# Kernel tuning notes

Measured on AMD Instinct MI355X. Metric: run time of the kernel, lower is better.

Reference implementation:

```python
import jax, jax.numpy as jnp
import numpy as np

N, INPUTDIM, OUTDIM, GRIDSIZE = 32768, 64, 256, 32


def setup_inputs() -> dict:
    key = jax.random.key(0)
    k1, k2 = jax.random.split(key)
    x = jax.random.normal(k1, (N, INPUTDIM), dtype=jnp.float32)
    # xavier_uniform over tensor of shape (2, outdim, inputdim, gridsize):
    # fan_in = inputdim*gridsize, fan_out = outdim*gridsize (torch treats dim0=fan_out-ish,
    # but exact init scale is irrelevant for correctness; use a matching uniform range)
    fan_in = INPUTDIM * GRIDSIZE
    fan_out = OUTDIM * GRIDSIZE
    bound = float(np.sqrt(6.0 / (fan_in + fan_out)))
    fouriercoeffs = jax.random.uniform(
        k2, (2, OUTDIM, INPUTDIM, GRIDSIZE), dtype=jnp.float32,
        minval=-bound, maxval=bound)
    bias = jnp.zeros((1, OUTDIM), dtype=jnp.float32)
    return {"x": x, "fouriercoeffs": fouriercoeffs, "bias": bias}


def reference(x, fouriercoeffs, bias):
    # gridsize_param rounds back to GRIDSIZE at init -> static.
    g = fouriercoeffs.shape[-1]
    k = jnp.arange(1, g + 1, dtype=x.dtype)  # (g,)
    # Fourier feature expansion: (N, inputdim, g)
    xk = x[:, :, None] * k[None, None, :]
    c = jnp.cos(xk)
    s = jnp.sin(xk)
    # Contract over (inputdim, gridsize) -> two GEMMs over flattened dim
    y = jnp.einsum('nig,oig->no', c, fouriercoeffs[0])
    y = y + jnp.einsum('nig,oig->no', s, fouriercoeffs[1])
    y = y + bias  # (1, outdim) broadcasts over N
    return y
```

## Files before the change

### kernel.cpp

```cpp
#include <hip/hip_runtime.h>


#define IDIM 64
#define ODIM 256
#define KDIM 4096
#define BM 128

typedef __attribute__((ext_vector_type(8))) unsigned short ushort8_t;
typedef __bf16 bf16x8 __attribute__((ext_vector_type(8)));
typedef float floatx4 __attribute__((ext_vector_type(4)));

__device__ __forceinline__ unsigned short f2bf_rne(float f) {
  unsigned int u = __float_as_uint(f);
  return (unsigned short)((u + 0x7FFFu + ((u >> 16) & 1u)) >> 16);
}

__device__ __forceinline__ void gl_lds16(const void* g, void* l) {
  __builtin_amdgcn_global_load_lds(
      (__attribute__((address_space(1))) void*)g,
      (__attribute__((address_space(3))) void*)l, 16, 0, 0);
}

__global__ void __launch_bounds__(256) wconv(const float* __restrict__ fc,
                                             unsigned short* __restrict__ Wr) {
  int e = (blockIdx.x * 256 + threadIdx.x) << 2;
  int o = e >> 12;
  int k = e & 4095;
  int i = k >> 6;
  int c = (k >> 5) & 1;
  int g = k & 31;
  const float4 v = *(const float4*)(fc + ((size_t)c << 19) + o * 2048 + i * 32 + g);
  ushort4 r;
  r.x = f2bf_rne(v.x);
  r.y = f2bf_rne(v.y);
  r.z = f2bf_rne(v.z);
  r.w = f2bf_rne(v.w);
  *(ushort4*)(Wr + e) = r;
}

__global__ void __launch_bounds__(512, 2) fkan_gemm(const float* __restrict__ X,
                                                    const unsigned short* __restrict__ Wr,
                                                    const float* __restrict__ bias,
                                                    float* __restrict__ out) {
  __shared__ __align__(16) unsigned char smem[98304];
  unsigned short* const AsBase = (unsigned short*)smem;
  unsigned short* const BsBase = (unsigned short*)(smem + 32768);

  const int t = threadIdx.x;
  const int wv = t >> 6;
  const int ln = t & 63;
  const int lm = ln & 15;
  const int quad = ln >> 4;
  const int wk = wv & 1;
  const int wn2 = (wv >> 1) & 1;
  const int wm2 = wv >> 2;
  const int m0 = blockIdx.x * BM;

  const int arow = t >> 2;
  const int q = t & 3;
  const float g0f = (float)(8 * q + 1);

  const int brow_off = ln >> 3;
  const int bchunk = (ln & 7) ^ (ln >> 3);
  const unsigned short* bsrc[4];
#pragma unroll
  for (int j = 0; j < 4; ++j)
    bsrc[j] = Wr + (size_t)(wv * 32 + j * 8 + brow_off) * KDIM + bchunk * 8;

  const int ga_c = arow * 8 + (q ^ (arow & 7));
  const int ga_s = arow * 8 + ((4 + q) ^ (arow & 7));

  floatx4 acc[4][8];
#pragma unroll
  for (int a = 0; a < 4; ++a)
#pragma unroll
    for (int b = 0; b < 8; ++b)
      acc[a][b] = (floatx4){0.0f, 0.0f, 0.0f, 0.0f};

  const float* xptr = X + (size_t)(m0 + arow) * IDIM;

  auto stageB = [&](int ktn, int buf) {
#pragma unroll
    for (int j = 0; j < 4; ++j)
      gl_lds16(bsrc[j] + ktn * 64, BsBase + buf * 16384 + (wv * 4 + j) * 512);
  };

  auto features = [&](float xv, int buf) {
    const float inv2pi = 0.15915494309189535f;
    float u = xv * inv2pi;
    float u0 = u * g0f;
    float c1 = __builtin_amdgcn_cosf(u);
    float s1 = __builtin_amdgcn_sinf(u);
    float C = __builtin_amdgcn_cosf(u0);
    float S = __builtin_amdgcn_sinf(u0);
    bf16x8 cb, sb;
    cb[0] = (__bf16)C;
    sb[0] = (__bf16)S;
#pragma unroll
    for (int j = 1; j < 8; ++j) {
      float Cn = __builtin_fmaf(C, c1, -(S * s1));
      float Sn = __builtin_fmaf(S, c1, (C * s1));
      C = Cn;
      S = Sn;
      cb[j] = (__bf16)C;
      sb[j] = (__bf16)S;
    }
    ushort8_t* As8 = (ushort8_t*)(AsBase + buf * 8192);
    As8[ga_c] = __builtin_bit_cast(ushort8_t, cb);
    As8[ga_s] = __builtin_bit_cast(ushort8_t, sb);
  };

  auto ktstep = [&](int ktn, int cur, int nxt) {
    float xn = xptr[ktn];
    stageB(ktn, nxt);

    const ushort8_t* A8 = (const ushort8_t*)(AsBase + cur * 8192);
    const ushort8_t* B8 = (const ushort8_t*)(BsBase + cur * 16384);
    const int ch = wk * 4 + quad;

    bf16x8 af[4], b0[4];
#pragma unroll
    for (int mt = 0; mt < 4; ++mt) {
      int r = wm2 * 64 + mt * 16 + lm;
      af[mt] = __builtin_bit_cast(bf16x8, A8[r * 8 + (ch ^ (r & 7))]);
    }
#pragma unroll
    for (int nt = 0; nt < 4; ++nt) {
      int n = wn2 * 128 + nt * 16 + lm;
      b0[nt] = __builtin_bit_cast(bf16x8, B8[n * 8 + (ch ^ (n & 7))]);
    }

    __builtin_amdgcn_s_setprio(1);
#pragma unroll
    for (int mt = 0; mt < 4; ++mt)
#pragma unroll
      for (int nt = 0; nt < 4; ++nt)
        acc[mt][nt] = __builtin_amdgcn_mfma_f32_16x16x32_bf16(
            af[mt], b0[nt], acc[mt][nt], 0, 0, 0);
    __builtin_amdgcn_s_setprio(0);

    features(xn, nxt);

    bf16x8 b1[4];
#pragma unroll
    for (int nt = 0; nt < 4; ++nt) {
      int n = wn2 * 128 + (nt + 4) * 16 + lm;
      b1[nt] = __builtin_bit_cast(bf16x8, B8[n * 8 + (ch ^ (n & 7))]);
    }

    __builtin_amdgcn_s_setprio(1);
#pragma unroll
    for (int mt = 0; mt < 4; ++mt)
#pragma unroll
      for (int nt = 0; nt < 4; ++nt)
        acc[mt][nt + 4] = __builtin_amdgcn_mfma_f32_16x16x32_bf16(
            af[mt], b1[nt], acc[mt][nt + 4], 0, 0, 0);
    __builtin_amdgcn_s_setprio(0);

    __syncthreads();
  };

  auto domfma = [&](int buf) {
    const ushort8_t* A8 = (const ushort8_t*)(AsBase + buf * 8192);
    const ushort8_t* B8 = (const ushort8_t*)(BsBase + buf * 16384);
    const int ch = wk * 4 + quad;
    bf16x8 af[4], bfr[8];
#pragma unroll
    for (int mt = 0; mt < 4; ++mt) {
      int r = wm2 * 64 + mt * 16 + lm;
      af[mt] = __builtin_bit_cast(bf16x8, A8[r * 8 + (ch ^ (r & 7))]);
    }
#pragma unroll
    for (int nt = 0; nt < 8; ++nt) {
      int n = wn2 * 128 + nt * 16 + lm;
      bfr[nt] = __builtin_bit_cast(bf16x8, B8[n * 8 + (ch ^ (n & 7))]);
    }
#pragma unroll
    for (int mt = 0; mt < 4; ++mt)
#pragma unroll
      for (int nt = 0; nt < 8; ++nt)
        acc[mt][nt] = __builtin_amdgcn_mfma_f32_16x16x32_bf16(
            af[mt], bfr[nt], acc[mt][nt], 0, 0, 0);
  };

  stageB(0, 0);
  features(xptr[0], 0);
  __syncthreads();

  for (int kt = 0; kt < 62; kt += 2) {
    ktstep(kt + 1, 0, 1);
    ktstep(kt + 2, 1, 0);
  }
  ktstep(63, 0, 1);
  domfma(1);

  float* red = (float*)smem;
  for (int half = 0; half < 2; ++half) {
    __syncthreads();
    if (wk == 1 && wm2 == half) {
#pragma unroll
      for (int mt = 0; mt < 4; ++mt)
#pragma unroll
        for (int nt = 0; nt < 8; ++nt) {
          int col = wn2 * 128 + nt * 16 + lm;
#pragma unroll
          for (int idx = 0; idx < 4; ++idx)
            red[(mt * 16 + quad * 4 + idx) * 260 + col] = acc[mt][nt][idx];
        }
    }
    __syncthreads();
    if (wk == 0 && wm2 == half) {
#pragma unroll
      for (int nt = 0; nt < 8; ++nt) {
        int col = wn2 * 128 + nt * 16 + lm;
        float bv = bias[col];
#pragma unroll
        for (int mt = 0; mt < 4; ++mt) {
          int rbase = m0 + half * 64 + mt * 16 + quad * 4;
#pragma unroll
          for (int idx = 0; idx < 4; ++idx)
            out[(size_t)(rbase + idx) * ODIM + col] =
                acc[mt][nt][idx] + red[(mt * 16 + quad * 4 + idx) * 260 + col] + bv;
        }
      }
    }
  }
}

extern "C" void kernel_launch(void* const* d_in, const int* in_sizes, int n_in,
                              void* d_out, int out_size, void* d_ws, size_t ws_size,
                              hipStream_t stream) {
  const float* x = (const float*)d_in[0];
  const float* fc = (const float*)d_in[1];
  const float* bias = (const float*)d_in[2];
  float* out = (float*)d_out;
  unsigned short* Wr = (unsigned short*)d_ws;

  hipLaunchKernelGGL(wconv, dim3(1024), dim3(256), 0, stream, fc, Wr);
  hipLaunchKernelGGL(fkan_gemm, dim3(256), dim3(512), 0, stream, x, Wr, bias, out);
}
```

Before: 140.6 us.

## Pre-swizzle weights into fragment order and load B directly into registers

The weight conversion kernel now writes bf16 weights in MFMA fragment order, so each wave reads its B operands straight from global memory into registers. This removes B staging through LDS and the matching LDS reads. The next k-step's B fragments are prefetched while the current MFMAs run. LDS use drops to the A double buffer plus a separate reduction buffer, which may allow higher occupancy. In exchange, more global/L2 traffic sits in the inner loop, and any L2 latency is now exposed to the MFMA stream.

```diff
diff --git a/kernel.cpp b/kernel.cpp
--- a/kernel.cpp
+++ b/kernel.cpp
@@ -15,36 +15,38 @@
   return (unsigned short)((u + 0x7FFFu + ((u >> 16) & 1u)) >> 16);
 }
 
-__device__ __forceinline__ void gl_lds16(const void* g, void* l) {
-  __builtin_amdgcn_global_load_lds(
-      (__attribute__((address_space(1))) void*)g,
-      (__attribute__((address_space(3))) void*)l, 16, 0, 0);
-}
-
 __global__ void __launch_bounds__(256) wconv(const float* __restrict__ fc,
                                              unsigned short* __restrict__ Wr) {
-  int e = (blockIdx.x * 256 + threadIdx.x) << 2;
-  int o = e >> 12;
-  int k = e & 4095;
-  int i = k >> 6;
-  int c = (k >> 5) & 1;
-  int g = k & 31;
-  const float4 v = *(const float4*)(fc + ((size_t)c << 19) + o * 2048 + i * 32 + g);
-  ushort4 r;
-  r.x = f2bf_rne(v.x);
-  r.y = f2bf_rne(v.y);
-  r.z = f2bf_rne(v.z);
-  r.w = f2bf_rne(v.w);
-  *(ushort4*)(Wr + e) = r;
+  int t = blockIdx.x * 256 + threadIdx.x;
+  int lane = t & 63;
+  int j = (t >> 6) & 7;
+  int bb = t >> 9;
+  int wn2 = bb & 1;
+  int wk = (bb >> 1) & 1;
+  int kt = bb >> 2;
+  int o = wn2 * 128 + j * 16 + (lane & 15);
+  int g0 = (lane >> 4) * 8;
+  const float* src = fc + ((size_t)wk << 19) + o * 2048 + kt * 32 + g0;
+  const float4 v0 = *(const float4*)(src);
+  const float4 v1 = *(const float4*)(src + 4);
+  ushort8_t r;
+  r[0] = f2bf_rne(v0.x);
+  r[1] = f2bf_rne(v0.y);
+  r[2] = f2bf_rne(v0.z);
+  r[3] = f2bf_rne(v0.w);
+  r[4] = f2bf_rne(v1.x);
+  r[5] = f2bf_rne(v1.y);
+  r[6] = f2bf_rne(v1.z);
+  r[7] = f2bf_rne(v1.w);
+  *(ushort8_t*)(Wr + (size_t)t * 8) = r;
 }
 
 __global__ void __launch_bounds__(512, 2) fkan_gemm(const float* __restrict__ X,
                                                     const unsigned short* __restrict__ Wr,
                                                     const float* __restrict__ bias,
                                                     float* __restrict__ out) {
-  __shared__ __align__(16) unsigned char smem[98304];
-  unsigned short* const AsBase = (unsigned short*)smem;
-  unsigned short* const BsBase = (unsigned short*)(smem + 32768);
+  __shared__ __align__(16) unsigned short As[2][8192];
+  __shared__ __align__(16) float red[64 * 260];
 
   const int t = threadIdx.x;
   const int wv = t >> 6;
@@ -60,16 +62,11 @@
   const int q = t & 3;
   const float g0f = (float)(8 * q + 1);
 
-  const int brow_off = ln >> 3;
-  const int bchunk = (ln & 7) ^ (ln >> 3);
-  const unsigned short* bsrc[4];
-#pragma unroll
-  for (int j = 0; j < 4; ++j)
-    bsrc[j] = Wr + (size_t)(wv * 32 + j * 8 + brow_off) * KDIM + bchunk * 8;
-
   const int ga_c = arow * 8 + (q ^ (arow & 7));
   const int ga_s = arow * 8 + ((4 + q) ^ (arow & 7));
 
+  const unsigned short* const bwave = Wr + (size_t)(wk * 2 + wn2) * 4096 + ln * 8;
+
   floatx4 acc[4][8];
 #pragma unroll
   for (int a = 0; a < 4; ++a)
@@ -78,12 +75,6 @@
       acc[a][b] = (floatx4){0.0f, 0.0f, 0.0f, 0.0f};
 
   const float* xptr = X + (size_t)(m0 + arow) * IDIM;
-
-  auto stageB = [&](int ktn, int buf) {
-#pragma unroll
-    for (int j = 0; j < 4; ++j)
-      gl_lds16(bsrc[j] + ktn * 64, BsBase + buf * 16384 + (wv * 4 + j) * 512);
-  };
 
   auto features = [&](float xv, int buf) {
     const float inv2pi = 0.15915494309189535f;
@@ -97,93 +88,70 @@
     cb[0] = (__bf16)C;
     sb[0] = (__bf16)S;
 #pragma unroll
-    for (int j = 1; j < 8; ++j) {
+    for (int jj = 1; jj < 8; ++jj) {
       float Cn = __builtin_fmaf(C, c1, -(S * s1));
       float Sn = __builtin_fmaf(S, c1, (C * s1));
       C = Cn;
       S = Sn;
-      cb[j] = (__bf16)C;
-      sb[j] = (__bf16)S;
-    }
-    ushort8_t* As8 = (ushort8_t*)(AsBase + buf * 8192);
+      cb[jj] = (__bf16)C;
+      sb[jj] = (__bf16)S;
+    }
+    ushort8_t* As8 = (ushort8_t*)As[buf];
     As8[ga_c] = __builtin_bit_cast(ushort8_t, cb);
     As8[ga_s] = __builtin_bit_cast(ushort8_t, sb);
   };
 
+  bf16x8 breg[8];
+
   auto ktstep = [&](int ktn, int cur, int nxt) {
     float xn = xptr[ktn];
-    stageB(ktn, nxt);
-
-    const ushort8_t* A8 = (const ushort8_t*)(AsBase + cur * 8192);
-    const ushort8_t* B8 = (const ushort8_t*)(BsBase + cur * 16384);
+    const ushort8_t* A8 = (const ushort8_t*)As[cur];
     const int ch = wk * 4 + quad;
-
-    bf16x8 af[4], b0[4];
+    bf16x8 af[4];
 #pragma unroll
     for (int mt = 0; mt < 4; ++mt) {
       int r = wm2 * 64 + mt * 16 + lm;
       af[mt] = __builtin_bit_cast(bf16x8, A8[r * 8 + (ch ^ (r & 7))]);
     }
-#pragma unroll
-    for (int nt = 0; nt < 4; ++nt) {
-      int n = wn2 * 128 + nt * 16 + lm;
-      b0[nt] = __builtin_bit_cast(bf16x8, B8[n * 8 + (ch ^ (n & 7))]);
-    }
+    const unsigned short* bn = bwave + (size_t)ktn * 16384;
 
     __builtin_amdgcn_s_setprio(1);
 #pragma unroll
-    for (int mt = 0; mt < 4; ++mt)
-#pragma unroll
-      for (int nt = 0; nt < 4; ++nt)
+    for (int nt = 0; nt < 8; ++nt) {
+#pragma unroll
+      for (int mt = 0; mt < 4; ++mt)
         acc[mt][nt] = __builtin_amdgcn_mfma_f32_16x16x32_bf16(
-            af[mt], b0[nt], acc[mt][nt], 0, 0, 0);
+            af[mt], breg[nt], acc[mt][nt], 0, 0, 0);
+      breg[nt] = __builtin_bit_cast(bf16x8, *(const ushort8_t*)(bn + nt * 512));
+    }
     __builtin_amdgcn_s_setprio(0);
 
     features(xn, nxt);
-
-    bf16x8 b1[4];
-#pragma unroll
-    for (int nt = 0; nt < 4; ++nt) {
-      int n = wn2 * 128 + (nt + 4) * 16 + lm;
-      b1[nt] = __builtin_bit_cast(bf16x8, B8[n * 8 + (ch ^ (n & 7))]);
-    }
-
-    __builtin_amdgcn_s_setprio(1);
-#pragma unroll
-    for (int mt = 0; mt < 4; ++mt)
-#pragma unroll
-      for (int nt = 0; nt < 4; ++nt)
-        acc[mt][nt + 4] = __builtin_amdgcn_mfma_f32_16x16x32_bf16(
-            af[mt], b1[nt], acc[mt][nt + 4], 0, 0, 0);
-    __builtin_amdgcn_s_setprio(0);
-
     __syncthreads();
   };
 
-  auto domfma = [&](int buf) {
-    const ushort8_t* A8 = (const ushort8_t*)(AsBase + buf * 8192);
-    const ushort8_t* B8 = (const ushort8_t*)(BsBase + buf * 16384);
+  auto ktlast = [&](int cur) {
+    const ushort8_t* A8 = (const ushort8_t*)As[cur];
     const int ch = wk * 4 + quad;
-    bf16x8 af[4], bfr[8];
+    bf16x8 af[4];
 #pragma unroll
     for (int mt = 0; mt < 4; ++mt) {
       int r = wm2 * 64 + mt * 16 + lm;
       af[mt] = __builtin_bit_cast(bf16x8, A8[r * 8 + (ch ^ (r & 7))]);
     }
-#pragma unroll
-    for (int nt = 0; nt < 8; ++nt) {
-      int n = wn2 * 128 + nt * 16 + lm;
-      bfr[nt] = __builtin_bit_cast(bf16x8, B8[n * 8 + (ch ^ (n & 7))]);
-    }
-#pragma unroll
-    for (int mt = 0; mt < 4; ++mt)
-#pragma unroll
-      for (int nt = 0; nt < 8; ++nt)
+    __builtin_amdgcn_s_setprio(1);
+#pragma unroll
+    for (int nt = 0; nt < 8; ++nt)
+#pragma unroll
+      for (int mt = 0; mt < 4; ++mt)
         acc[mt][nt] = __builtin_amdgcn_mfma_f32_16x16x32_bf16(
-            af[mt], bfr[nt], acc[mt][nt], 0, 0, 0);
+            af[mt], breg[nt], acc[mt][nt], 0, 0, 0);
+    __builtin_amdgcn_s_setprio(0);
   };
 
-  stageB(0, 0);
+#pragma unroll
+  for (int nt = 0; nt < 8; ++nt)
+    breg[nt] = __builtin_bit_cast(bf16x8, *(const ushort8_t*)(bwave + nt * 512));
   features(xptr[0], 0);
   __syncthreads();
 
@@ -192,9 +160,8 @@
     ktstep(kt + 2, 1, 0);
   }
   ktstep(63, 0, 1);
-  domfma(1);
-
-  float* red = (float*)smem;
+  ktlast(1);
+
   for (int half = 0; half < 2; ++half) {
     __syncthreads();
     if (wk == 1 && wm2 == half) {
@@ -236,6 +203,6 @@
   float* out = (float*)d_out;
   unsigned short* Wr = (unsigned short*)d_ws;
 
-  hipLaunchKernelGGL(wconv, dim3(1024), dim3(256), 0, stream, fc, Wr);
+  hipLaunchKernelGGL(wconv, dim3(512), dim3(256), 0, stream, fc, Wr);
   hipLaunchKernelGGL(fkan_gemm, dim3(256), dim3(512), 0, stream, x, Wr, bias, out);
 }
```

Result: faster. 132.6 us (-5.7%).
